# Performance work log

Hardware: AMD Instinct MI355X
Metric: run time of the kernel (lower is better)

Reference implementation:

```python
import jax, jax.numpy as jnp
import numpy as np

H = 16
D = 64  # head_dim = 1024 // 16
SCALE = D ** -0.5


def setup_inputs() -> dict:
    key = jax.random.key(0)
    ks = jax.random.split(key, 12)
    B, N, C = 2, 2048, 1024
    s = C ** -0.5
    return {
        "hidden_states": jax.random.normal(ks[0], (B, N, C), jnp.float32),
        "pos_embeds": jax.random.normal(ks[1], (B, N, C), jnp.float32),
        "Wq": jax.random.normal(ks[2], (C, C), jnp.float32) * s,
        "bq": jnp.zeros((C,), jnp.float32),
        "Wk": jax.random.normal(ks[3], (C, C), jnp.float32) * s,
        "bk": jnp.zeros((C,), jnp.float32),
        "Wv": jax.random.normal(ks[4], (C, C), jnp.float32) * s,
        "bv": jnp.zeros((C,), jnp.float32),
        "Wpos": jax.random.normal(ks[5], (C, C), jnp.float32) * s,
        "pos_bias_u": jax.random.normal(ks[6], (H, D), jnp.float32) * 0.1,
        "pos_bias_v": jax.random.normal(ks[7], (H, D), jnp.float32) * 0.1,
        "Wo": jax.random.normal(ks[8], (C, C), jnp.float32) * s,
        "bo": jnp.zeros((C,), jnp.float32),
    }


def reference(hidden_states, pos_embeds, Wq, bq, Wk, bk, Wv, bv, Wpos,
              pos_bias_u, pos_bias_v, Wo, bo):
    B, N, C = hidden_states.shape
    # projections (torch Linear: y = x @ W.T + b), split heads -> (B, N, H, D)
    q = (hidden_states @ Wq.T + bq).reshape(B, N, H, D)
    k = (hidden_states @ Wk.T + bk).reshape(B, N, H, D)
    v = (hidden_states @ Wv.T + bv).reshape(B, N, H, D)
    p = (pos_embeds @ Wpos.T).reshape(B, N, H, D)
    # relative-position biased logits: matrix_ac + matrix_bd
    q_u = q + pos_bias_u  # (B,N,H,D) + (H,D)
    q_v = q + pos_bias_v
    ac = jnp.einsum('bnhd,bmhd->bhnm', q_u, k)
    bd = jnp.einsum('bnhd,bmhd->bhnm', q_v, p)
    attn = jax.nn.softmax((ac + bd) * SCALE, axis=-1)  # (B,H,N,N)
    out = jnp.einsum('bhnm,bmhd->bnhd', attn, v).reshape(B, N, C)
    return out @ Wo.T + bo
```

## Files before the change

### kernel.cpp

```cpp
#include <hip/hip_runtime.h>
#include <hip/hip_bf16.h>


typedef short bf16x8 __attribute__((ext_vector_type(8)));
typedef float f32x4 __attribute__((ext_vector_type(4)));

#define BB 2
#define NN 2048
#define CC 1024
#define HH 16
#define DD 64
#define MM (BB * NN)
#define SC2E 0.18033688f

__device__ __forceinline__ unsigned short f2bf(float f) {
    union { float f; unsigned int u; } x; x.f = f;
    unsigned int r = x.u + 0x7FFFu + ((x.u >> 16) & 1u);
    return (unsigned short)(r >> 16);
}

__device__ __forceinline__ float bf2f(unsigned short s) {
    union { unsigned int u; float f; } x; x.u = ((unsigned int)s) << 16;
    return x.f;
}

__device__ __forceinline__ unsigned int pk2(float a, float b) {
    __hip_bfloat162 h = __float22bfloat162_rn(make_float2(a, b));
    unsigned int u; __builtin_memcpy(&u, &h, 4); return u;
}

typedef __attribute__((address_space(1))) const unsigned int* gas1_t;
typedef __attribute__((address_space(3))) unsigned int* las3_t;

__device__ __forceinline__ void gload_lds16(const unsigned short* g, unsigned short* l) {
    __builtin_amdgcn_global_load_lds((gas1_t)g, (las3_t)l, 16, 0, 0);
}

__global__ __launch_bounds__(256) void compute_wuv(const float* __restrict__ Wk,
                                                   const float* __restrict__ Wpos,
                                                   const float* __restrict__ pbu,
                                                   const float* __restrict__ pbv,
                                                   const float* __restrict__ bk,
                                                   unsigned short* __restrict__ wkpb,
                                                   float* __restrict__ cub) {
    const int gid = blockIdx.x * 256 + threadIdx.x;
    const int h = gid >> 11;
    const int col = gid & 2047;
    const float* Wsrc = (col < 1024) ? Wk : Wpos;
    const float* uv = (col < 1024) ? pbu : pbv;
    const int c = col & 1023;
    float acc = 0.f;
#pragma unroll 8
    for (int d = 0; d < 64; ++d)
        acc += uv[h * 64 + d] * Wsrc[(size_t)(h * 64 + d) * 1024 + c];
    wkpb[(size_t)(1024 + h) * 2048 + col] = f2bf(acc * SC2E);
    if (gid < 16) {
        float s = 0.f;
        for (int d = 0; d < 64; ++d) s += pbu[gid * 64 + d] * bk[gid * 64 + d];
        cub[gid] = s * SC2E;
    }
}

struct CastArgs {
    const float* src[7];
    unsigned short* dst[7];
    int stride[7];
    int colOff[7];
    int n4[7];
};
__global__ __launch_bounds__(256) void cast_all(CastArgs a) {
    const int seg = blockIdx.y;
    const int i = blockIdx.x * 256 + threadIdx.x;
    if (i >= a.n4[seg]) return;
    float4 v = ((const float4*)a.src[seg])[i];
    uint2 u;
    u.x = pk2(v.x, v.y);
    u.y = pk2(v.z, v.w);
    const int row = i >> 8, c4 = (i & 255) * 4;
    *(uint2*)&a.dst[seg][(size_t)row * a.stride[seg] + a.colOff[seg] + c4] = u;
}

struct GemmBatch {
    const unsigned short* A[3];
    const unsigned short* B[3];
    unsigned short* out[3];
    const float* bias[3];
    int lda[3], ldb[3], Kz[3];
    float* cbp;
    const float* cub;
};
__global__ __launch_bounds__(256) void gemm_qkvp(GemmBatch g) {
    __shared__ unsigned short Sh[2 * 128 * 64];
    unsigned short* As = Sh;
    unsigned short* Bs = Sh + 128 * 64;
    const int z = blockIdx.z;
    if (z != 1 && blockIdx.y == 8) return;
    const unsigned short* __restrict__ A = g.A[z];
    const unsigned short* __restrict__ B = g.B[z];
    unsigned short* __restrict__ out = g.out[z];
    const float* __restrict__ bias = g.bias[z];
    const int lda = g.lda[z], ldb = g.ldb[z], K = g.Kz[z];

    const int t = threadIdx.x;
    const int w = t >> 6, lane = t & 63, l15 = lane & 15, quad = lane >> 4;
    const int m0 = blockIdx.x * 128, n0 = blockIdx.y * 128;
    const int wm = (w >> 1) * 64, wn = (w & 1) * 64;

    f32x4 acc[4][4];
#pragma unroll
    for (int i = 0; i < 4; ++i)
#pragma unroll
        for (int j = 0; j < 4; ++j)
#pragma unroll
            for (int r = 0; r < 4; ++r) acc[i][j][r] = 0.f;

    for (int kb = 0; kb < K; kb += 64) {
        __syncthreads();
#pragma unroll
        for (int j = 0; j < 4; ++j) {
            const int id = j * 256 + t;
            const int half = id >> 9;
            const int id9 = id & 511;
            const int row = id9 >> 2, c4 = (id9 & 3) * 8;
            gload_lds16(&A[(size_t)(m0 + row) * lda + kb + half * 32 + c4],
                        &As[half * 4096 + id9 * 8]);
            gload_lds16(&B[(size_t)(n0 + row) * ldb + kb + half * 32 + c4],
                        &Bs[half * 4096 + id9 * 8]);
        }
        __syncthreads();
#pragma unroll
        for (int kk = 0; kk < 2; ++kk) {
            bf16x8 af[4], bfr[4];
#pragma unroll
            for (int i = 0; i < 4; ++i)
                af[i] = *(const bf16x8*)&As[kk * 4096 + (wm + i * 16 + l15) * 32 + quad * 8];
#pragma unroll
            for (int j = 0; j < 4; ++j)
                bfr[j] = *(const bf16x8*)&Bs[kk * 4096 + (wn + j * 16 + l15) * 32 + quad * 8];
#pragma unroll
            for (int i = 0; i < 4; ++i)
#pragma unroll
                for (int j = 0; j < 4; ++j)
                    acc[i][j] = __builtin_amdgcn_mfma_f32_16x16x32_bf16(af[i], bfr[j], acc[i][j], 0, 0, 0);
        }
    }

    if (z == 1 && n0 == 1024) {
        if ((w & 1) == 0) {
            const int bI = (m0 + wm) >> 11;
            const int nbase = (m0 + wm) & 2047;
            const float cu = g.cub[l15];
#pragma unroll
            for (int i = 0; i < 4; ++i)
#pragma unroll
                for (int r = 0; r < 4; ++r) {
                    const int nseq = nbase + i * 16 + quad * 4 + r;
                    g.cbp[((size_t)(bI * 16 + l15)) * 2048 + nseq] = acc[i][0][r] + cu;
                }
        }
    } else if (z != 2) {
        const float sc = (z == 0) ? SC2E : 1.f;
#pragma unroll
        for (int i = 0; i < 4; ++i)
#pragma unroll
            for (int j = 0; j < 4; ++j) {
                const int col = n0 + wn + j * 16 + l15;
                const int row_base = m0 + wm + i * 16 + quad * 4;
                const float bc = bias ? bias[col] : 0.f;
#pragma unroll
                for (int r = 0; r < 4; ++r)
                    out[(size_t)(row_base + r) * CC + col] = f2bf((acc[i][j][r] + bc) * sc);
            }
    } else {
        __syncthreads();
        unsigned short* Tr = &Sh[w * 1152];
        const int bI = (m0 + wm) >> 11, nseq0 = (m0 + wm) & 2047;
        const int colL = lane >> 3;
        const int mL = (lane & 7) * 8;
#pragma unroll
        for (int j = 0; j < 4; ++j) {
            const int col = n0 + wn + j * 16 + l15;
            const float bc = bias[col];
#pragma unroll
            for (int i = 0; i < 4; ++i) {
                uint2 pk;
                pk.x = pk2(acc[i][j][0] + bc, acc[i][j][1] + bc);
                pk.y = pk2(acc[i][j][2] + bc, acc[i][j][3] + bc);
                *(uint2*)&Tr[l15 * 72 + i * 16 + quad * 4] = pk;
            }
#pragma unroll
            for (int p = 0; p < 2; ++p) {
                const int cl = p * 8 + colL;
                uint4 vv = *(const uint4*)&Tr[cl * 72 + mL];
                const int gcol = n0 + wn + j * 16 + cl;
                const int hh = gcol >> 6, dd = gcol & 63;
                *(uint4*)&out[((size_t)(bI * 16 + hh) * 64 + dd) * 2048 + nseq0 + mL] = vv;
            }
        }
    }
}

__global__ __launch_bounds__(512) void attn_kernel(const unsigned short* __restrict__ q,
                                                   const unsigned short* __restrict__ kp,
                                                   const unsigned short* __restrict__ vt,
                                                   const float* __restrict__ cb,
                                                   unsigned short* __restrict__ att) {
    __shared__ unsigned short Ks[2][128 * 64];
    __shared__ unsigned short Vs[2][64 * 128];
    __shared__ unsigned short Ps[8][16 * 64];

    const int t = threadIdx.x;
    const int w = t >> 6, lane = t & 63, l15 = lane & 15, quad = lane >> 4;
    const int qt = blockIdx.x, h = blockIdx.y, b = blockIdx.z;
    const int e3 = l15 & 7;

    bf16x8 qf[2];
    {
        const int qrow = qt * 128 + w * 16 + l15;
        const size_t qoff = ((size_t)(b * NN + qrow) * HH + h) * DD;
#pragma unroll
        for (int c2 = 0; c2 < 2; ++c2)
            qf[c2] = *(const bf16x8*)&q[qoff + c2 * 32 + quad * 8];
    }

    f32x4 oT[4];
    float l_lane = 0.f;
#pragma unroll
    for (int db = 0; db < 4; ++db)
#pragma unroll
        for (int r = 0; r < 4; ++r) oT[db][r] = 0.f;

    const size_t kbase = (size_t)b * NN * CC + (size_t)h * DD;
    const size_t vbase = (size_t)(b * HH + h) * DD * NN;
    const size_t cbase = (size_t)(b * HH + h) * NN;

    int krow[2], kgc[2], vd[2], vgc[2];
#pragma unroll
    for (int j = 0; j < 2; ++j) {
        const int id = j * 512 + t;
        krow[j] = id >> 3;
        kgc[j] = ((id & 7) ^ (krow[j] & 7)) * 8;
        vd[j] = id >> 4;
        vgc[j] = ((id & 15) ^ (vd[j] & 7)) * 8;
    }

#pragma unroll
    for (int j = 0; j < 2; ++j) {
        const int id = j * 512 + t;
        gload_lds16(&kp[kbase + (size_t)krow[j] * CC + kgc[j]], &Ks[0][id * 8]);
        gload_lds16(&vt[vbase + (size_t)vd[j] * NN + vgc[j]], &Vs[0][id * 8]);
    }

    for (int kt = 0; kt < NN / 128; ++kt) {
        const int cur = kt & 1;
        __syncthreads();
        if (kt + 1 < NN / 128) {
#pragma unroll
            for (int j = 0; j < 2; ++j) {
                const int id = j * 512 + t;
                gload_lds16(&kp[kbase + (size_t)((kt + 1) * 128 + krow[j]) * CC + kgc[j]],
                            &Ks[cur ^ 1][id * 8]);
                gload_lds16(&vt[vbase + (size_t)vd[j] * NN + (kt + 1) * 128 + vgc[j]],
                            &Vs[cur ^ 1][id * 8]);
            }
        }

        f32x4 c8r[8];
#pragma unroll
        for (int t8 = 0; t8 < 8; ++t8)
            c8r[t8] = *(const f32x4*)&cb[cbase + kt * 128 + t8 * 16 + quad * 4];

#pragma unroll
        for (int half = 0; half < 2; ++half) {
            f32x4 s[4];
#pragma unroll
            for (int t4 = 0; t4 < 4; ++t4) s[t4] = c8r[half * 4 + t4];

            __builtin_amdgcn_s_setprio(1);
#pragma unroll
            for (int t4 = 0; t4 < 4; ++t4) {
                const int row = half * 64 + t4 * 16 + l15;
#pragma unroll
                for (int c2 = 0; c2 < 2; ++c2) {
                    bf16x8 kf = *(const bf16x8*)&Ks[cur][row * 64 + (((c2 * 4 + quad) ^ e3) * 8)];
                    s[t4] = __builtin_amdgcn_mfma_f32_16x16x32_bf16(kf, qf[c2], s[t4], 0, 0, 0);
                }
            }
            __builtin_amdgcn_s_setprio(0);

            float rs = 0.f;
#pragma unroll
            for (int t4 = 0; t4 < 4; ++t4)
#pragma unroll
                for (int r = 0; r < 4; ++r) {
                    float pv = exp2f(s[t4][r]);
                    s[t4][r] = pv;
                    rs += pv;
                }
            l_lane += rs;
#pragma unroll
            for (int t4 = 0; t4 < 4; ++t4) {
                uint2 pk;
                pk.x = pk2(s[t4][0], s[t4][1]);
                pk.y = pk2(s[t4][2], s[t4][3]);
                const int blk = t4 * 2 + (quad >> 1);
                *(uint2*)&Ps[w][l15 * 64 + ((blk ^ e3) * 8) + (quad & 1) * 4] = pk;
            }

            __builtin_amdgcn_s_setprio(1);
#pragma unroll
            for (int c2 = 0; c2 < 2; ++c2) {
                bf16x8 pf = *(const bf16x8*)&Ps[w][l15 * 64 + (((c2 * 4 + quad) ^ e3) * 8)];
#pragma unroll
                for (int db = 0; db < 4; ++db) {
                    bf16x8 vf = *(const bf16x8*)&Vs[cur][(db * 16 + l15) * 128 +
                                                         (((half * 8 + c2 * 4 + quad) ^ e3) * 8)];
                    oT[db] = __builtin_amdgcn_mfma_f32_16x16x32_bf16(vf, pf, oT[db], 0, 0, 0);
                }
            }
            __builtin_amdgcn_s_setprio(0);
        }
    }

    float l = l_lane;
    l += __shfl_xor(l, 16);
    l += __shfl_xor(l, 32);
    const float inv = 1.f / l;
    const int qrow = qt * 128 + w * 16 + l15;
    const size_t ob = ((size_t)(b * NN + qrow) * HH + h) * DD;
#pragma unroll
    for (int db = 0; db < 4; ++db) {
        uint2 pk;
        pk.x = pk2(oT[db][0] * inv, oT[db][1] * inv);
        pk.y = pk2(oT[db][2] * inv, oT[db][3] * inv);
        *(uint2*)&att[ob + db * 16 + quad * 4] = pk;
    }
}

__global__ __launch_bounds__(256) void gemm_out(const unsigned short* __restrict__ A,
                                                const unsigned short* __restrict__ B,
                                                float* __restrict__ out,
                                                const float* __restrict__ bias) {
    constexpr int K = CC;
    __shared__ unsigned short As[128 * 32];
    __shared__ unsigned short Bs[64 * 32];
    const int t = threadIdx.x;
    const int w = t >> 6, lane = t & 63, l15 = lane & 15, quad = lane >> 4;
    const int m0 = blockIdx.x * 128, n0 = blockIdx.y * 64;
    const int wm = (w >> 1) * 64, wn = (w & 1) * 32;

    f32x4 acc[4][2];
#pragma unroll
    for (int i = 0; i < 4; ++i)
#pragma unroll
        for (int j = 0; j < 2; ++j)
#pragma unroll
            for (int r = 0; r < 4; ++r) acc[i][j][r] = 0.f;

    for (int kb = 0; kb < K; kb += 32) {
        __syncthreads();
#pragma unroll
        for (int j = 0; j < 2; ++j) {
            int id = j * 256 + t;
            int row = id >> 2, c4 = (id & 3) * 8;
            gload_lds16(&A[(size_t)(m0 + row) * K + kb + c4], &As[id * 8]);
        }
        {
            int row = t >> 2, c4 = (t & 3) * 8;
            gload_lds16(&B[(size_t)(n0 + row) * K + kb + c4], &Bs[t * 8]);
        }
        __syncthreads();
        bf16x8 af[4], bfr[2];
#pragma unroll
        for (int i = 0; i < 4; ++i)
            af[i] = *(const bf16x8*)&As[(wm + i * 16 + l15) * 32 + quad * 8];
#pragma unroll
        for (int j = 0; j < 2; ++j)
            bfr[j] = *(const bf16x8*)&Bs[(wn + j * 16 + l15) * 32 + quad * 8];
#pragma unroll
        for (int i = 0; i < 4; ++i)
#pragma unroll
            for (int j = 0; j < 2; ++j)
                acc[i][j] = __builtin_amdgcn_mfma_f32_16x16x32_bf16(af[i], bfr[j], acc[i][j], 0, 0, 0);
    }

#pragma unroll
    for (int i = 0; i < 4; ++i)
#pragma unroll
        for (int j = 0; j < 2; ++j) {
            const int col = n0 + wn + j * 16 + l15;
            const int row_base = m0 + wm + i * 16 + quad * 4;
            const float bc = bias[col];
#pragma unroll
            for (int r = 0; r < 4; ++r)
                out[(size_t)(row_base + r) * CC + col] = acc[i][j][r] + bc;
        }
}

extern "C" void kernel_launch(void* const* d_in, const int* in_sizes, int n_in,
                              void* d_out, int out_size, void* d_ws, size_t ws_size,
                              hipStream_t stream) {
    const float* hs   = (const float*)d_in[0];
    const float* pos  = (const float*)d_in[1];
    const float* Wq   = (const float*)d_in[2];
    const float* bq   = (const float*)d_in[3];
    const float* Wk   = (const float*)d_in[4];
    const float* bk   = (const float*)d_in[5];
    const float* Wv   = (const float*)d_in[6];
    const float* bv   = (const float*)d_in[7];
    const float* Wpos = (const float*)d_in[8];
    const float* pbu  = (const float*)d_in[9];
    const float* pbv  = (const float*)d_in[10];
    const float* Wo   = (const float*)d_in[11];
    const float* bo   = (const float*)d_in[12];
    float* out = (float*)d_out;

    const size_t nHS = (size_t)MM * CC;
    const size_t nW  = (size_t)CC * CC;

    unsigned short* p = (unsigned short*)d_ws;
    unsigned short* hspb = p;            p += (size_t)MM * 2048;
    unsigned short* wqb  = p;            p += nW;
    unsigned short* wkpb = p;            p += (size_t)1152 * 2048;
    unsigned short* wvb  = p;            p += nW;
    unsigned short* wob  = p;            p += nW;
    unsigned short* qsb  = p;            p += nHS;
    unsigned short* kpb  = p;            p += nHS;
    unsigned short* vtb  = p;            p += nHS;
    float* cb  = (float*)p;              p += (size_t)BB * HH * NN * 2;
    float* cub = (float*)p;              p += 32;
    unsigned short* attb = hspb;

    compute_wuv<<<128, 256, 0, stream>>>(Wk, Wpos, pbu, pbv, bk, wkpb, cub);

    CastArgs ca;
    ca.src[0] = hs;   ca.dst[0] = hspb; ca.stride[0] = 2048; ca.colOff[0] = 0;    ca.n4[0] = (int)(nHS / 4);
    ca.src[1] = pos;  ca.dst[1] = hspb; ca.stride[1] = 2048; ca.colOff[1] = 1024; ca.n4[1] = (int)(nHS / 4);
    ca.src[2] = Wq;   ca.dst[2] = wqb;  ca.stride[2] = 1024; ca.colOff[2] = 0;    ca.n4[2] = (int)(nW / 4);
    ca.src[3] = Wk;   ca.dst[3] = wkpb; ca.stride[3] = 2048; ca.colOff[3] = 0;    ca.n4[3] = (int)(nW / 4);
    ca.src[4] = Wpos; ca.dst[4] = wkpb; ca.stride[4] = 2048; ca.colOff[4] = 1024; ca.n4[4] = (int)(nW / 4);
    ca.src[5] = Wv;   ca.dst[5] = wvb;  ca.stride[5] = 1024; ca.colOff[5] = 0;    ca.n4[5] = (int)(nW / 4);
    ca.src[6] = Wo;   ca.dst[6] = wob;  ca.stride[6] = 1024; ca.colOff[6] = 0;    ca.n4[6] = (int)(nW / 4);
    dim3 cgrid((unsigned)(nHS / 4 / 256), 7);
    cast_all<<<cgrid, 256, 0, stream>>>(ca);

    GemmBatch gb;
    gb.A[0] = hspb; gb.lda[0] = 2048; gb.B[0] = wqb;  gb.ldb[0] = 1024; gb.Kz[0] = 1024; gb.out[0] = qsb; gb.bias[0] = bq;
    gb.A[1] = hspb; gb.lda[1] = 2048; gb.B[1] = wkpb; gb.ldb[1] = 2048; gb.Kz[1] = 2048; gb.out[1] = kpb; gb.bias[1] = bk;
    gb.A[2] = hspb; gb.lda[2] = 2048; gb.B[2] = wvb;  gb.ldb[2] = 1024; gb.Kz[2] = 1024; gb.out[2] = vtb; gb.bias[2] = bv;
    gb.cbp = cb; gb.cub = cub;
    dim3 ggrid(MM / 128, 9, 3);
    gemm_qkvp<<<ggrid, 256, 0, stream>>>(gb);

    dim3 agrid(NN / 128, HH, BB);
    attn_kernel<<<agrid, 512, 0, stream>>>(qsb, kpb, vtb, cb, attb);

    dim3 ogrid(MM / 128, CC / 64);
    gemm_out<<<ogrid, 256, 0, stream>>>(attb, wob, out, bo);
}
```

Measured before the change: 267.1 us.

## Flatten QKV-pos GEMM grid and use narrower tiles for the K=2048 projection

Replaces the 3D grid, which left early-exit blocks idle, with a flat 1056-block schedule. The long-K key/pos projection is split into 128x64 tiles, giving it twice as many blocks so the work per block is more even. The cb (pos-bias) slice keeps its own block kind. The aim is better load balance and fewer wasted blocks across the CUs, at the cost of lower arithmetic intensity for the narrow tiles and more branchy code.

New measurement: 284.5 us. 1.07x slower.

```diff
diff --git a/kernel.cpp b/kernel.cpp
--- a/kernel.cpp
+++ b/kernel.cpp
@@ -81,11 +81,16 @@
 }
 
 struct GemmBatch {
-    const unsigned short* A[3];
-    const unsigned short* B[3];
-    unsigned short* out[3];
-    const float* bias[3];
-    int lda[3], ldb[3], Kz[3];
+    const unsigned short* hsp;
+    const unsigned short* wq;
+    const unsigned short* wkp;
+    const unsigned short* wv;
+    unsigned short* q;
+    unsigned short* kp;
+    unsigned short* vt;
+    const float* bq;
+    const float* bk;
+    const float* bv;
     float* cbp;
     const float* cub;
 };
@@ -93,18 +98,24 @@
     __shared__ unsigned short Sh[2 * 128 * 64];
     unsigned short* As = Sh;
     unsigned short* Bs = Sh + 128 * 64;
-    const int z = blockIdx.z;
-    if (z != 1 && blockIdx.y == 8) return;
-    const unsigned short* __restrict__ A = g.A[z];
-    const unsigned short* __restrict__ B = g.B[z];
-    unsigned short* __restrict__ out = g.out[z];
-    const float* __restrict__ bias = g.bias[z];
-    const int lda = g.lda[z], ldb = g.ldb[z], K = g.Kz[z];
+
+    const int bid = blockIdx.x;
+    int kind, m0, n0, K;
+    if (bid < 256)       { kind = 0; m0 = (bid & 31) * 128;  n0 = (bid >> 5) * 128; K = 1024; }
+    else if (bid < 768)  { int i2 = bid - 256;  kind = 1; m0 = (i2 & 31) * 128; n0 = (i2 >> 5) * 64; K = 2048; }
+    else if (bid < 1024) { int i3 = bid - 768;  kind = 2; m0 = (i3 & 31) * 128; n0 = (i3 >> 5) * 128; K = 1024; }
+    else                 { int i4 = bid - 1024; kind = 3; m0 = i4 * 128;        n0 = 1024;            K = 2048; }
+    const bool wide = (kind == 0) || (kind == 2);
+
+    const unsigned short* __restrict__ A = g.hsp;
+    const unsigned short* __restrict__ B = (kind == 0) ? g.wq : (kind == 2) ? g.wv : g.wkp;
+    const int lda = 2048, ldb = wide ? ((kind == 0) ? 1024 : 1024) : 2048;
 
     const int t = threadIdx.x;
     const int w = t >> 6, lane = t & 63, l15 = lane & 15, quad = lane >> 4;
-    const int m0 = blockIdx.x * 128, n0 = blockIdx.y * 128;
-    const int wm = (w >> 1) * 64, wn = (w & 1) * 64;
+    const int wm = (w >> 1) * 64;
+    const int wn = wide ? (w & 1) * 64 : (w & 1) * 32;
+    const int NJ = wide ? 4 : 2;
 
     f32x4 acc[4][4];
 #pragma unroll
@@ -119,13 +130,29 @@
 #pragma unroll
         for (int j = 0; j < 4; ++j) {
             const int id = j * 256 + t;
-            const int half = id >> 9;
-            const int id9 = id & 511;
+            const int half = id >> 9, id9 = id & 511;
             const int row = id9 >> 2, c4 = (id9 & 3) * 8;
             gload_lds16(&A[(size_t)(m0 + row) * lda + kb + half * 32 + c4],
                         &As[half * 4096 + id9 * 8]);
-            gload_lds16(&B[(size_t)(n0 + row) * ldb + kb + half * 32 + c4],
-                        &Bs[half * 4096 + id9 * 8]);
+        }
+        if (wide) {
+#pragma unroll
+            for (int j = 0; j < 4; ++j) {
+                const int id = j * 256 + t;
+                const int half = id >> 9, id9 = id & 511;
+                const int row = id9 >> 2, c4 = (id9 & 3) * 8;
+                gload_lds16(&B[(size_t)(n0 + row) * ldb + kb + half * 32 + c4],
+                            &Bs[half * 4096 + id9 * 8]);
+            }
+        } else {
+#pragma unroll
+            for (int j = 0; j < 2; ++j) {
+                const int id = j * 256 + t;
+                const int half = id >> 8, id8 = id & 255;
+                const int row = id8 >> 2, c4 = (id8 & 3) * 8;
+                gload_lds16(&B[(size_t)(n0 + row) * ldb + kb + half * 32 + c4],
+                            &Bs[half * 2048 + id8 * 8]);
+            }
         }
         __syncthreads();
 #pragma unroll
@@ -134,18 +161,53 @@
 #pragma unroll
             for (int i = 0; i < 4; ++i)
                 af[i] = *(const bf16x8*)&As[kk * 4096 + (wm + i * 16 + l15) * 32 + quad * 8];
-#pragma unroll
-            for (int j = 0; j < 4; ++j)
-                bfr[j] = *(const bf16x8*)&Bs[kk * 4096 + (wn + j * 16 + l15) * 32 + quad * 8];
-#pragma unroll
-            for (int i = 0; i < 4; ++i)
+            if (wide) {
 #pragma unroll
                 for (int j = 0; j < 4; ++j)
-                    acc[i][j] = __builtin_amdgcn_mfma_f32_16x16x32_bf16(af[i], bfr[j], acc[i][j], 0, 0, 0);
-        }
-    }
-
-    if (z == 1 && n0 == 1024) {
+                    bfr[j] = *(const bf16x8*)&Bs[kk * 4096 + (wn + j * 16 + l15) * 32 + quad * 8];
+#pragma unroll
+                for (int i = 0; i < 4; ++i)
+#pragma unroll
+                    for (int j = 0; j < 4; ++j)
+                        acc[i][j] = __builtin_amdgcn_mfma_f32_16x16x32_bf16(af[i], bfr[j], acc[i][j], 0, 0, 0);
+            } else {
+#pragma unroll
+                for (int j = 0; j < 2; ++j)
+                    bfr[j] = *(const bf16x8*)&Bs[kk * 2048 + (wn + j * 16 + l15) * 32 + quad * 8];
+#pragma unroll
+                for (int i = 0; i < 4; ++i)
+#pragma unroll
+                    for (int j = 0; j < 2; ++j)
+                        acc[i][j] = __builtin_amdgcn_mfma_f32_16x16x32_bf16(af[i], bfr[j], acc[i][j], 0, 0, 0);
+            }
+        }
+    }
+
+    if (kind == 0) {
+#pragma unroll
+        for (int i = 0; i < 4; ++i)
+#pragma unroll
+            for (int j = 0; j < 4; ++j) {
+                const int col = n0 + wn + j * 16 + l15;
+                const int row_base = m0 + wm + i * 16 + quad * 4;
+                const float bc = g.bq[col];
+#pragma unroll
+                for (int r = 0; r < 4; ++r)
+                    g.q[(size_t)(row_base + r) * CC + col] = f2bf((acc[i][j][r] + bc) * SC2E);
+            }
+    } else if (kind == 1) {
+#pragma unroll
+        for (int i = 0; i < 4; ++i)
+#pragma unroll
+            for (int j = 0; j < 2; ++j) {
+                const int col = n0 + wn + j * 16 + l15;
+                const int row_base = m0 + wm + i * 16 + quad * 4;
+                const float bc = g.bk[col];
+#pragma unroll
+                for (int r = 0; r < 4; ++r)
+                    g.kp[(size_t)(row_base + r) * CC + col] = f2bf(acc[i][j][r] + bc);
+            }
+    } else if (kind == 3) {
         if ((w & 1) == 0) {
             const int bI = (m0 + wm) >> 11;
             const int nbase = (m0 + wm) & 2047;
@@ -158,19 +220,6 @@
                     g.cbp[((size_t)(bI * 16 + l15)) * 2048 + nseq] = acc[i][0][r] + cu;
                 }
         }
-    } else if (z != 2) {
-        const float sc = (z == 0) ? SC2E : 1.f;
-#pragma unroll
-        for (int i = 0; i < 4; ++i)
-#pragma unroll
-            for (int j = 0; j < 4; ++j) {
-                const int col = n0 + wn + j * 16 + l15;
-                const int row_base = m0 + wm + i * 16 + quad * 4;
-                const float bc = bias ? bias[col] : 0.f;
-#pragma unroll
-                for (int r = 0; r < 4; ++r)
-                    out[(size_t)(row_base + r) * CC + col] = f2bf((acc[i][j][r] + bc) * sc);
-            }
     } else {
         __syncthreads();
         unsigned short* Tr = &Sh[w * 1152];
@@ -180,7 +229,7 @@
 #pragma unroll
         for (int j = 0; j < 4; ++j) {
             const int col = n0 + wn + j * 16 + l15;
-            const float bc = bias[col];
+            const float bc = g.bv[col];
 #pragma unroll
             for (int i = 0; i < 4; ++i) {
                 uint2 pk;
@@ -194,7 +243,7 @@
                 uint4 vv = *(const uint4*)&Tr[cl * 72 + mL];
                 const int gcol = n0 + wn + j * 16 + cl;
                 const int hh = gcol >> 6, dd = gcol & 63;
-                *(uint4*)&out[((size_t)(bI * 16 + hh) * 64 + dd) * 2048 + nseq0 + mL] = vv;
+                *(uint4*)&g.vt[((size_t)(bI * 16 + hh) * 64 + dd) * 2048 + nseq0 + mL] = vv;
             }
         }
     }
@@ -445,12 +494,11 @@
     cast_all<<<cgrid, 256, 0, stream>>>(ca);
 
     GemmBatch gb;
-    gb.A[0] = hspb; gb.lda[0] = 2048; gb.B[0] = wqb;  gb.ldb[0] = 1024; gb.Kz[0] = 1024; gb.out[0] = qsb; gb.bias[0] = bq;
-    gb.A[1] = hspb; gb.lda[1] = 2048; gb.B[1] = wkpb; gb.ldb[1] = 2048; gb.Kz[1] = 2048; gb.out[1] = kpb; gb.bias[1] = bk;
-    gb.A[2] = hspb; gb.lda[2] = 2048; gb.B[2] = wvb;  gb.ldb[2] = 1024; gb.Kz[2] = 1024; gb.out[2] = vtb; gb.bias[2] = bv;
+    gb.hsp = hspb; gb.wq = wqb; gb.wkp = wkpb; gb.wv = wvb;
+    gb.q = qsb; gb.kp = kpb; gb.vt = vtb;
+    gb.bq = bq; gb.bk = bk; gb.bv = bv;
     gb.cbp = cb; gb.cub = cub;
-    dim3 ggrid(MM / 128, 9, 3);
-    gemm_qkvp<<<ggrid, 256, 0, stream>>>(gb);
+    gemm_qkvp<<<1056, 256, 0, stream>>>(gb);
 
     dim3 agrid(NN / 128, HH, BB);
     attn_kernel<<<agrid, 512, 0, stream>>>(qsb, kpb, vtb, cb, attb);
```
